# Kernel optimization log

Measured on AMD Instinct MI355X. Metric: run time of the kernel, lower is better.

The kernel has to match this reference:

```python
import jax, jax.numpy as jnp
import numpy as np

MARGIN = 1.0


def _rand_offdiag(key, n):
    # uniform random index j != k for each row k (replaces Python random.choice)
    j = jax.random.randint(key, (n,), 0, n - 1)
    return j + (j >= jnp.arange(n)).astype(j.dtype)


def _semi_hard_margin_loss(logits, j_rand, j_fallback, margin):
    # logits: [N, N]; anchor for row k is logits[k, k]
    n = logits.shape[0]
    rows = jnp.arange(n)
    anchor = jnp.diagonal(logits)                      # [N]
    # term 1: random imposter, hinge at 0 (loss added only when diff > 0)
    imp1 = logits[rows, j_rand]
    d1 = jnp.maximum(imp1 - anchor + margin, 0.0)
    # term 2: semi-hard imposter = max over entries strictly below the anchor
    neg_inf = jnp.finfo(logits.dtype).min
    mask = logits < anchor[:, None]                    # diagonal never True
    cand_max = jnp.max(jnp.where(mask, logits, neg_inf), axis=1)
    has_cand = jnp.any(mask, axis=1)
    imp2 = jnp.where(has_cand, cand_max, logits[rows, j_fallback])
    d2 = jnp.maximum(imp2 - anchor + margin, 0.0)
    return jnp.mean(d1 + d2)


def setup_inputs() -> dict:
    key = jax.random.key(0)
    kx, ky = jax.random.split(key)
    x = jax.random.normal(kx, (4096, 1024), dtype=jnp.float32)
    y = jax.random.normal(ky, (4096, 1024), dtype=jnp.float32)
    return {"x": x, "y": y}


def reference(x, y):
    logits = jnp.matmul(x, y.T)                        # [N, N]
    n = logits.shape[0]
    k1, k2, k3, k4 = jax.random.split(jax.random.key(42), 4)
    loss = (_semi_hard_margin_loss(logits, _rand_offdiag(k1, n), _rand_offdiag(k2, n), MARGIN)
            + _semi_hard_margin_loss(logits.T, _rand_offdiag(k3, n), _rand_offdiag(k4, n), MARGIN))
    return loss
```

## Files before the change

kernel.cpp:

```cpp
#include <hip/hip_runtime.h>
#include <stdint.h>
#include <stddef.h>

#define NN 4096
#define KK 1024
#define SPAN 4095u

typedef unsigned short ushort_t;
typedef __attribute__((ext_vector_type(8))) short short8v;
typedef __attribute__((ext_vector_type(4))) float f32x4;

__host__ __device__ inline void tf2x32(uint32_t k0, uint32_t k1,
                                       uint32_t x0, uint32_t x1,
                                       uint32_t* o0, uint32_t* o1) {
  uint32_t ks2 = k0 ^ k1 ^ 0x1BD11BDAu;
  uint32_t v0 = x0 + k0;
  uint32_t v1 = x1 + k1;
#define TF_ROT(x, r) (((x) << (r)) | ((x) >> (32 - (r))))
#define TF_RND(r) do { v0 += v1; v1 = TF_ROT(v1, r); v1 ^= v0; } while (0)
  TF_RND(13); TF_RND(15); TF_RND(26); TF_RND(6);
  v0 += k1;  v1 += ks2 + 1u;
  TF_RND(17); TF_RND(29); TF_RND(16); TF_RND(24);
  v0 += ks2; v1 += k0 + 2u;
  TF_RND(13); TF_RND(15); TF_RND(26); TF_RND(6);
  v0 += k0;  v1 += k1 + 3u;
  TF_RND(17); TF_RND(29); TF_RND(16); TF_RND(24);
  v0 += k1;  v1 += ks2 + 4u;
  TF_RND(13); TF_RND(15); TF_RND(26); TF_RND(6);
  v0 += ks2; v1 += k0 + 5u;
#undef TF_RND
#undef TF_ROT
  *o0 = v0; *o1 = v1;
}

__device__ inline uint32_t rb32(uint32_t ka, uint32_t kb, uint32_t i) {
  uint32_t a, b;
  tf2x32(ka, kb, 0u, i, &a, &b);
  return a ^ b;
}

__device__ inline uint32_t fenc(float f) {
  uint32_t b = __float_as_uint(f);
  return (b & 0x80000000u) ? ~b : (b | 0x80000000u);
}
__device__ inline float fdec(uint32_t e) {
  uint32_t b = (e & 0x80000000u) ? (e & 0x7FFFFFFFu) : ~e;
  return __uint_as_float(b);
}

__device__ inline ushort_t bf16rne(float f) {
  uint32_t u = __float_as_uint(f);
  return (ushort_t)((u + 0x7FFFu + ((u >> 16) & 1u)) >> 16);
}

__device__ inline void glds16(const void* g, void* l) {
  __builtin_amdgcn_global_load_lds((const __attribute__((address_space(1))) void*)g,
                                   (__attribute__((address_space(3))) void*)l, 16, 0, 0);
}

__global__ __launch_bounds__(256) void k_front(
    const float* __restrict__ X, const float* __restrict__ Y,
    ushort_t* __restrict__ Xb, ushort_t* __restrict__ Yb,
    uint32_t s0a, uint32_t s0b, uint32_t s1a, uint32_t s1b,
    uint32_t s2a, uint32_t s2b, uint32_t s3a, uint32_t s3b,
    uint32_t* __restrict__ rowmax, uint32_t* __restrict__ colmax,
    float* __restrict__ anchor, float* __restrict__ irr, float* __restrict__ irf,
    float* __restrict__ icr, float* __restrict__ icf) {
  const int b = blockIdx.x, tid = threadIdx.x;

  if (b < 4096) {
    if (b < 16) rowmax[b * 256 + tid] = 0u;
    else if (b < 32) colmax[(b - 16) * 256 + tid] = 0u;
    const float4* src = (const float4*)((b < 2048) ? X : Y);
    ushort4* dst = (ushort4*)((b < 2048) ? Xb : Yb);
    const int n4 = NN * KK / 4;
    for (int i = (b & 2047) * 256 + tid; i < n4; i += 2048 * 256) {
      float4 v = src[i];
      ushort4 o;
      o.x = bf16rne(v.x); o.y = bf16rne(v.y); o.z = bf16rne(v.z); o.w = bf16rne(v.w);
      dst[i] = o;
    }
    return;
  }

  const int wid = tid >> 6;
  const int lane = tid & 63;
  const int row = (b - 4096) * 4 + wid;

  int jl = 0;
  if (lane < 4) {
    uint32_t ka = (lane == 0) ? s0a : (lane == 1) ? s1a : (lane == 2) ? s2a : s3a;
    uint32_t kb = (lane == 0) ? s0b : (lane == 1) ? s1b : (lane == 2) ? s2b : s3b;
    uint32_t k1a, k1b, k2a, k2b;
    tf2x32(ka, kb, 0u, 0u, &k1a, &k1b);
    tf2x32(ka, kb, 0u, 1u, &k2a, &k2b);
    uint32_t hi = rb32(k1a, k1b, (uint32_t)row);
    uint32_t lo = rb32(k2a, k2b, (uint32_t)row);
    uint32_t off = ((hi % SPAN) * 256u + (lo % SPAN)) % SPAN;
    int j = (int)off;
    jl = j + ((j >= row) ? 1 : 0);
  }
  const int j1r = __shfl(jl, 0), j1f = __shfl(jl, 1);
  const int j2r = __shfl(jl, 2), j2f = __shfl(jl, 3);

  const float4* xk = (const float4*)(X + (size_t)row * KK);
  const float4* yk = (const float4*)(Y + (size_t)row * KK);
  const float4* y1 = (const float4*)(Y + (size_t)j1r * KK);
  const float4* y2 = (const float4*)(Y + (size_t)j1f * KK);
  const float4* x1 = (const float4*)(X + (size_t)j2r * KK);
  const float4* x2 = (const float4*)(X + (size_t)j2f * KK);
  float sa = 0.f, s1 = 0.f, s2 = 0.f, s3 = 0.f, s4 = 0.f;
  for (int t = lane; t < KK / 4; t += 64) {
    float4 xv = xk[t], yv = yk[t], a1 = y1[t], a2 = y2[t], b1 = x1[t], b2 = x2[t];
    sa = fmaf(xv.x, yv.x, fmaf(xv.y, yv.y, fmaf(xv.z, yv.z, fmaf(xv.w, yv.w, sa))));
    s1 = fmaf(xv.x, a1.x, fmaf(xv.y, a1.y, fmaf(xv.z, a1.z, fmaf(xv.w, a1.w, s1))));
    s2 = fmaf(xv.x, a2.x, fmaf(xv.y, a2.y, fmaf(xv.z, a2.z, fmaf(xv.w, a2.w, s2))));
    s3 = fmaf(b1.x, yv.x, fmaf(b1.y, yv.y, fmaf(b1.z, yv.z, fmaf(b1.w, yv.w, s3))));
    s4 = fmaf(b2.x, yv.x, fmaf(b2.y, yv.y, fmaf(b2.z, yv.z, fmaf(b2.w, yv.w, s4))));
  }
  for (int m = 32; m >= 1; m >>= 1) {
    sa += __shfl_xor(sa, m);
    s1 += __shfl_xor(s1, m);
    s2 += __shfl_xor(s2, m);
    s3 += __shfl_xor(s3, m);
    s4 += __shfl_xor(s4, m);
  }
  if (lane == 0) {
    anchor[row] = sa; irr[row] = s1; irf[row] = s2; icr[row] = s3; icf[row] = s4;
  }
}

__global__ __launch_bounds__(512, 2) void k_gemm8p(
    const ushort_t* __restrict__ A, const ushort_t* __restrict__ B,
    const float* __restrict__ anchor,
    uint32_t* __restrict__ rowmax, uint32_t* __restrict__ colmax) {
  __shared__ ushort_t AL[2][2][8192];
  __shared__ ushort_t BL[2][2][8192];

  const int tid = threadIdx.x;
  const int lane = tid & 63;
  const int w = tid >> 6, wr = w >> 2, wc = w & 3;
  const int l15 = lane & 15, l4 = lane >> 4;

  const int swz = (blockIdx.x & 7) * 32 + (blockIdx.x >> 3);
  const int bi = swz >> 4, bj = swz & 15;

  const int strow = tid >> 3;
  const int scol = ((tid & 7) ^ (strow & 7)) * 8;
  const ushort_t* Abase = A + (size_t)(bi * 256 + strow) * KK + scol;
  const ushort_t* Bbase = B + (size_t)(bj * 256 + strow) * KK + scol;

  const int ss0 = ((0 * 4 + l4) ^ (l15 & 7)) * 8;
  const int ss1 = ((1 * 4 + l4) ^ (l15 & 7)) * 8;
  const int bhalf = wc >> 1, brow0 = (wc & 1) * 64 + l15;

  f32x4 acc[8][4] = {};
  short8v Areg[4][2], B0r[2][2], B1r[2][2];

#define STAGE_A(DD, KT)                                                        \
  do {                                                                         \
    glds16(Abase + (size_t)0 * KK + (KT) * 64,   &AL[DD][0][tid * 8]);         \
    glds16(Abase + (size_t)64 * KK + (KT) * 64,  &AL[DD][0][4096 + tid * 8]);  \
    glds16(Abase + (size_t)128 * KK + (KT) * 64, &AL[DD][1][tid * 8]);         \
    glds16(Abase + (size_t)192 * KK + (KT) * 64, &AL[DD][1][4096 + tid * 8]);  \
  } while (0)
#define STAGE_B(DD, KT)                                                        \
  do {                                                                         \
    glds16(Bbase + (size_t)0 * KK + (KT) * 64,   &BL[DD][0][tid * 8]);         \
    glds16(Bbase + (size_t)64 * KK + (KT) * 64,  &BL[DD][0][4096 + tid * 8]);  \
    glds16(Bbase + (size_t)128 * KK + (KT) * 64, &BL[DD][1][tid * 8]);         \
    glds16(Bbase + (size_t)192 * KK + (KT) * 64, &BL[DD][1][4096 + tid * 8]);  \
  } while (0)

#define BAR() do { __builtin_amdgcn_s_barrier(); \
                   __builtin_amdgcn_sched_barrier(0); } while (0)
#define LGKM0() do { asm volatile("s_waitcnt lgkmcnt(0)" ::: "memory"); \
                     __builtin_amdgcn_sched_barrier(0); } while (0)
#define VM8BAR() do { asm volatile("s_waitcnt vmcnt(8)" ::: "memory"); \
                      __builtin_amdgcn_s_barrier(); \
                      __builtin_amdgcn_sched_barrier(0); } while (0)

#define MFMA1(a, b, c) c = __builtin_amdgcn_mfma_f32_16x16x32_bf16(a, b, c, 0, 0, 0)
#define CL16(MS, NS, BR)                                                       \
  do {                                                                         \
    __builtin_amdgcn_s_setprio(1);                                             \
    _Pragma("unroll")                                                          \
    for (int q = 0; q < 4; ++q) {                                              \
      MFMA1(Areg[q][0], BR[0][0], acc[(MS) * 4 + q][(NS) * 2]);                \
      MFMA1(Areg[q][0], BR[1][0], acc[(MS) * 4 + q][(NS) * 2 + 1]);            \
      MFMA1(Areg[q][1], BR[0][1], acc[(MS) * 4 + q][(NS) * 2]);                \
      MFMA1(Areg[q][1], BR[1][1], acc[(MS) * 4 + q][(NS) * 2 + 1]);            \
    }                                                                          \
    __builtin_amdgcn_s_setprio(0);                                             \
  } while (0)

#define LDA(D, M, KH) (*(const short8v*)&AL[D][wr][((M) * 16 + l15) * 64 + ((KH) ? ss1 : ss0)])
#define LDB(D, N, KH) (*(const short8v*)&BL[D][bhalf][(brow0 + (N) * 16) * 64 + ((KH) ? ss1 : ss0)])

  STAGE_B(0, 0); STAGE_A(0, 0);
  STAGE_B(1, 1); STAGE_A(1, 1);
  asm volatile("s_waitcnt vmcnt(8)" ::: "memory");
  __builtin_amdgcn_s_barrier();
  __builtin_amdgcn_sched_barrier(0);

  for (int i = 0; i < 8; ++i) {
    const int kt2 = (2 * i + 2) & 15, kt3 = (2 * i + 3) & 15;

#pragma unroll
    for (int q = 0; q < 4; ++q) { Areg[q][0] = LDA(0, q, 0); Areg[q][1] = LDA(0, q, 1); }
#pragma unroll
    for (int n = 0; n < 2; ++n) { B0r[n][0] = LDB(0, n, 0); B0r[n][1] = LDB(0, n, 1); }
    BAR(); LGKM0();
    CL16(0, 0, B0r);
    BAR();

#pragma unroll
    for (int n = 0; n < 2; ++n) { B1r[n][0] = LDB(0, n + 2, 0); B1r[n][1] = LDB(0, n + 2, 1); }
    BAR(); LGKM0();
    CL16(0, 1, B1r);
    BAR();

#pragma unroll
    for (int q = 0; q < 4; ++q) { Areg[q][0] = LDA(0, q + 4, 0); Areg[q][1] = LDA(0, q + 4, 1); }
    STAGE_B(0, kt2);
    BAR(); LGKM0();
    CL16(1, 1, B1r);
    BAR();

    STAGE_A(0, kt2);
    BAR(); LGKM0();
    CL16(1, 0, B0r);
    VM8BAR();

#pragma unroll
    for (int q = 0; q < 4; ++q) { Areg[q][0] = LDA(1, q, 0); Areg[q][1] = LDA(1, q, 1); }
#pragma unroll
    for (int n = 0; n < 2; ++n) { B0r[n][0] = LDB(1, n, 0); B0r[n][1] = LDB(1, n, 1); }
    BAR(); LGKM0();
    CL16(0, 0, B0r);
    BAR();

#pragma unroll
    for (int n = 0; n < 2; ++n) { B1r[n][0] = LDB(1, n + 2, 0); B1r[n][1] = LDB(1, n + 2, 1); }
    BAR(); LGKM0();
    CL16(0, 1, B1r);
    BAR();

#pragma unroll
    for (int q = 0; q < 4; ++q) { Areg[q][0] = LDA(1, q + 4, 0); Areg[q][1] = LDA(1, q + 4, 1); }
    STAGE_B(1, kt3);
    BAR(); LGKM0();
    CL16(1, 1, B1r);
    BAR();

    STAGE_A(1, kt3);
    BAR(); LGKM0();
    CL16(1, 0, B0r);
    VM8BAR();
  }

#undef LDA
#undef LDB
#undef CL16
#undef MFMA1
#undef VM8BAR
#undef LGKM0
#undef BAR
#undef STAGE_A
#undef STAGE_B

  const int rbase = bi * 256 + wr * 128;
  const int cbase = bj * 256 + wc * 64;

  float ar[32], ac[4];
#pragma unroll
  for (int m = 0; m < 8; ++m)
#pragma unroll
    for (int r = 0; r < 4; ++r)
      ar[m * 4 + r] = anchor[rbase + m * 16 + l4 * 4 + r];
#pragma unroll
  for (int n = 0; n < 4; ++n)
    ac[n] = anchor[cbase + n * 16 + l15];

#pragma unroll
  for (int m = 0; m < 8; ++m) {
#pragma unroll
    for (int r = 0; r < 4; ++r) {
      const int rg = rbase + m * 16 + l4 * 4 + r;
      const float a = ar[m * 4 + r];
      uint32_t e = 0;
#pragma unroll
      for (int n = 0; n < 4; ++n) {
        const int cg = cbase + n * 16 + l15;
        float v = acc[m][n][r];
        if (v < a && rg != cg) { uint32_t fe = fenc(v); e = (fe > e) ? fe : e; }
      }
#pragma unroll
      for (int sh = 1; sh < 16; sh <<= 1) {
        uint32_t o = (uint32_t)__shfl_xor((int)e, sh, 64);
        e = (o > e) ? o : e;
      }
      if (l15 == 0 && e) atomicMax(&rowmax[rg], e);
    }
  }
#pragma unroll
  for (int n = 0; n < 4; ++n) {
    const int cg = cbase + n * 16 + l15;
    const float a = ac[n];
    uint32_t e = 0;
#pragma unroll
    for (int m = 0; m < 8; ++m) {
#pragma unroll
      for (int r = 0; r < 4; ++r) {
        const int rg = rbase + m * 16 + l4 * 4 + r;
        float v = acc[m][n][r];
        if (v < a && rg != cg) { uint32_t fe = fenc(v); e = (fe > e) ? fe : e; }
      }
    }
    {
      uint32_t o = (uint32_t)__shfl_xor((int)e, 16, 64); e = (o > e) ? o : e;
      o = (uint32_t)__shfl_xor((int)e, 32, 64);          e = (o > e) ? o : e;
    }
    if (l4 == 0 && e) atomicMax(&colmax[cg], e);
  }
}

__global__ __launch_bounds__(256) void k_final(
    const float* __restrict__ anchor,
    const float* __restrict__ irr, const float* __restrict__ irf,
    const float* __restrict__ icr, const float* __restrict__ icf,
    const uint32_t* __restrict__ rowmax, const uint32_t* __restrict__ colmax,
    float* __restrict__ out) {
  float s = 0.f;
  for (int k = (int)threadIdx.x; k < NN; k += 256) {
    float a = anchor[k];
    float d1 = fmaxf(irr[k] - a + 1.0f, 0.f);
    uint32_t rm = rowmax[k];
    float imp2r = rm ? fdec(rm) : irf[k];
    float d2 = fmaxf(imp2r - a + 1.0f, 0.f);
    float e1 = fmaxf(icr[k] - a + 1.0f, 0.f);
    uint32_t cm = colmax[k];
    float imp2c = cm ? fdec(cm) : icf[k];
    float e2 = fmaxf(imp2c - a + 1.0f, 0.f);
    s += d1 + d2 + e1 + e2;
  }
  __shared__ float red[4];
  for (int m = 32; m >= 1; m >>= 1) s += __shfl_xor(s, m);
  if ((threadIdx.x & 63) == 0) red[threadIdx.x >> 6] = s;
  __syncthreads();
  if (threadIdx.x == 0) out[0] = (red[0] + red[1] + red[2] + red[3]) * (1.0f / NN);
}

extern "C" void kernel_launch(void* const* d_in, const int* in_sizes, int n_in,
                              void* d_out, int out_size, void* d_ws, size_t ws_size,
                              hipStream_t stream) {
  const float* X = (const float*)d_in[0];
  const float* Y = (const float*)d_in[1];
  float* out = (float*)d_out;

  char* ws = (char*)d_ws;
  float* anchor    = (float*)(ws + 0 * 16384);
  float* irr       = (float*)(ws + 1 * 16384);
  float* irf       = (float*)(ws + 2 * 16384);
  float* icr       = (float*)(ws + 3 * 16384);
  float* icf       = (float*)(ws + 4 * 16384);
  uint32_t* rowmax = (uint32_t*)(ws + 5 * 16384);
  uint32_t* colmax = (uint32_t*)(ws + 6 * 16384);
  ushort_t* Xb     = (ushort_t*)(ws + 256 * 1024);
  ushort_t* Yb     = Xb + (size_t)NN * KK;

  uint32_t sk[4][2];
  for (int i = 0; i < 4; ++i) tf2x32(0u, 42u, 0u, (uint32_t)i, &sk[i][0], &sk[i][1]);

  k_front<<<4096 + NN / 4, 256, 0, stream>>>(
      X, Y, Xb, Yb,
      sk[0][0], sk[0][1], sk[1][0], sk[1][1], sk[2][0], sk[2][1], sk[3][0], sk[3][1],
      rowmax, colmax, anchor, irr, irf, icr, icf);

  k_gemm8p<<<256, 512, 0, stream>>>(Xb, Yb, anchor, rowmax, colmax);

  k_final<<<1, 256, 0, stream>>>(anchor, irr, irf, icr, icf, rowmax, colmax, out);
}
```

Baseline: 94.20 us.

## Use four waves per 256x256 tile with 128x128 per-wave subtiles

The GEMM block drops from 512 threads (8 waves, each computing 128x64) to 256 threads (4 waves, each computing 128x128), with correspondingly more staging loads per thread and a restructured per-k-tile MFMA schedule. Each wave now holds 64 accumulator tiles and reuses each A and B fragment across more MFMAs, which reduces LDS reads per flop. In exchange, register pressure roughly doubles, occupancy drops to one block with four waves per CU, and there are fewer waves available to hide latency.

Result: slower. 141.5 us (+50.2%).

```diff
diff --git a/kernel.cpp b/kernel.cpp
--- a/kernel.cpp
+++ b/kernel.cpp
@@ -130,7 +130,7 @@
   }
 }
 
-__global__ __launch_bounds__(512, 2) void k_gemm8p(
+__global__ __launch_bounds__(256, 1) void k_gemm4w(
     const ushort_t* __restrict__ A, const ushort_t* __restrict__ B,
     const float* __restrict__ anchor,
     uint32_t* __restrict__ rowmax, uint32_t* __restrict__ colmax) {
@@ -139,7 +139,7 @@
 
   const int tid = threadIdx.x;
   const int lane = tid & 63;
-  const int w = tid >> 6, wr = w >> 2, wc = w & 3;
+  const int w = tid >> 6, wr = w >> 1, wc = w & 1;
   const int l15 = lane & 15, l4 = lane >> 4;
 
   const int swz = (blockIdx.x & 7) * 32 + (blockIdx.x >> 3);
@@ -147,139 +147,131 @@
 
   const int strow = tid >> 3;
   const int scol = ((tid & 7) ^ (strow & 7)) * 8;
-  const ushort_t* Abase = A + (size_t)(bi * 256 + strow) * KK + scol;
-  const ushort_t* Bbase = B + (size_t)(bj * 256 + strow) * KK + scol;
+  const ushort_t* Ab0 = A + (size_t)(bi * 256 + strow) * KK + scol;
+  const ushort_t* Ab1 = A + (size_t)(bi * 256 + 128 + strow) * KK + scol;
+  const ushort_t* Bb0 = B + (size_t)(bj * 256 + strow) * KK + scol;
+  const ushort_t* Bb1 = B + (size_t)(bj * 256 + 128 + strow) * KK + scol;
 
   const int ss0 = ((0 * 4 + l4) ^ (l15 & 7)) * 8;
   const int ss1 = ((1 * 4 + l4) ^ (l15 & 7)) * 8;
-  const int bhalf = wc >> 1, brow0 = (wc & 1) * 64 + l15;
-
-  f32x4 acc[8][4] = {};
-  short8v Areg[4][2], B0r[2][2], B1r[2][2];
+
+  f32x4 acc[8][8] = {};
+  short8v Areg[8], B0r[4], B1r[4];
 
 #define STAGE_A(DD, KT)                                                        \
   do {                                                                         \
-    glds16(Abase + (size_t)0 * KK + (KT) * 64,   &AL[DD][0][tid * 8]);         \
-    glds16(Abase + (size_t)64 * KK + (KT) * 64,  &AL[DD][0][4096 + tid * 8]);  \
-    glds16(Abase + (size_t)128 * KK + (KT) * 64, &AL[DD][1][tid * 8]);         \
-    glds16(Abase + (size_t)192 * KK + (KT) * 64, &AL[DD][1][4096 + tid * 8]);  \
+    glds16(Ab0 + (size_t)0 * KK + (KT) * 64,   &AL[DD][0][0 * 2048 + tid * 8]);\
+    glds16(Ab0 + (size_t)32 * KK + (KT) * 64,  &AL[DD][0][1 * 2048 + tid * 8]);\
+    glds16(Ab0 + (size_t)64 * KK + (KT) * 64,  &AL[DD][0][2 * 2048 + tid * 8]);\
+    glds16(Ab0 + (size_t)96 * KK + (KT) * 64,  &AL[DD][0][3 * 2048 + tid * 8]);\
+    glds16(Ab1 + (size_t)0 * KK + (KT) * 64,   &AL[DD][1][0 * 2048 + tid * 8]);\
+    glds16(Ab1 + (size_t)32 * KK + (KT) * 64,  &AL[DD][1][1 * 2048 + tid * 8]);\
+    glds16(Ab1 + (size_t)64 * KK + (KT) * 64,  &AL[DD][1][2 * 2048 + tid * 8]);\
+    glds16(Ab1 + (size_t)96 * KK + (KT) * 64,  &AL[DD][1][3 * 2048 + tid * 8]);\
   } while (0)
 #define STAGE_B(DD, KT)                                                        \
   do {                                                                         \
-    glds16(Bbase + (size_t)0 * KK + (KT) * 64,   &BL[DD][0][tid * 8]);         \
-    glds16(Bbase + (size_t)64 * KK + (KT) * 64,  &BL[DD][0][4096 + tid * 8]);  \
-    glds16(Bbase + (size_t)128 * KK + (KT) * 64, &BL[DD][1][tid * 8]);         \
-    glds16(Bbase + (size_t)192 * KK + (KT) * 64, &BL[DD][1][4096 + tid * 8]);  \
+    glds16(Bb0 + (size_t)0 * KK + (KT) * 64,   &BL[DD][0][0 * 2048 + tid * 8]);\
+    glds16(Bb0 + (size_t)32 * KK + (KT) * 64,  &BL[DD][0][1 * 2048 + tid * 8]);\
+    glds16(Bb0 + (size_t)64 * KK + (KT) * 64,  &BL[DD][0][2 * 2048 + tid * 8]);\
+    glds16(Bb0 + (size_t)96 * KK + (KT) * 64,  &BL[DD][0][3 * 2048 + tid * 8]);\
+    glds16(Bb1 + (size_t)0 * KK + (KT) * 64,   &BL[DD][1][0 * 2048 + tid * 8]);\
+    glds16(Bb1 + (size_t)32 * KK + (KT) * 64,  &BL[DD][1][1 * 2048 + tid * 8]);\
+    glds16(Bb1 + (size_t)64 * KK + (KT) * 64,  &BL[DD][1][2 * 2048 + tid * 8]);\
+    glds16(Bb1 + (size_t)96 * KK + (KT) * 64,  &BL[DD][1][3 * 2048 + tid * 8]);\
   } while (0)
 
 #define BAR() do { __builtin_amdgcn_s_barrier(); \
                    __builtin_amdgcn_sched_barrier(0); } while (0)
 #define LGKM0() do { asm volatile("s_waitcnt lgkmcnt(0)" ::: "memory"); \
                      __builtin_amdgcn_sched_barrier(0); } while (0)
-#define VM8BAR() do { asm volatile("s_waitcnt vmcnt(8)" ::: "memory"); \
-                      __builtin_amdgcn_s_barrier(); \
-                      __builtin_amdgcn_sched_barrier(0); } while (0)
+#define VM16BAR() do { asm volatile("s_waitcnt vmcnt(16)" ::: "memory"); \
+                       __builtin_amdgcn_s_barrier(); \
+                       __builtin_amdgcn_sched_barrier(0); } while (0)
+
+#define RD_A(D, KH)                                                            \
+  do {                                                                         \
+    _Pragma("unroll")                                                          \
+    for (int q = 0; q < 8; ++q)                                                \
+      Areg[q] = *(const short8v*)&AL[D][wr][(q * 16 + l15) * 64                \
+                                            + ((KH) ? ss1 : ss0)];             \
+  } while (0)
+#define RD_B(RR, D, NB, KH)                                                    \
+  do {                                                                         \
+    _Pragma("unroll")                                                          \
+    for (int n = 0; n < 4; ++n)                                                \
+      RR[n] = *(const short8v*)&BL[D][wc][(((NB) * 4 + n) * 16 + l15) * 64     \
+                                          + ((KH) ? ss1 : ss0)];               \
+  } while (0)
 
 #define MFMA1(a, b, c) c = __builtin_amdgcn_mfma_f32_16x16x32_bf16(a, b, c, 0, 0, 0)
-#define CL16(MS, NS, BR)                                                       \
+#define CL32(BR, NB)                                                           \
   do {                                                                         \
     __builtin_amdgcn_s_setprio(1);                                             \
     _Pragma("unroll")                                                          \
-    for (int q = 0; q < 4; ++q) {                                              \
-      MFMA1(Areg[q][0], BR[0][0], acc[(MS) * 4 + q][(NS) * 2]);                \
-      MFMA1(Areg[q][0], BR[1][0], acc[(MS) * 4 + q][(NS) * 2 + 1]);            \
-      MFMA1(Areg[q][1], BR[0][1], acc[(MS) * 4 + q][(NS) * 2]);                \
-      MFMA1(Areg[q][1], BR[1][1], acc[(MS) * 4 + q][(NS) * 2 + 1]);            \
+    for (int q = 0; q < 8; ++q) {                                              \
+      MFMA1(Areg[q], BR[0], acc[q][(NB) * 4 + 0]);                             \
+      MFMA1(Areg[q], BR[1], acc[q][(NB) * 4 + 1]);                             \
+      MFMA1(Areg[q], BR[2], acc[q][(NB) * 4 + 2]);                             \
+      MFMA1(Areg[q], BR[3], acc[q][(NB) * 4 + 3]);                             \
     }                                                                          \
     __builtin_amdgcn_s_setprio(0);                                             \
   } while (0)
 
-#define LDA(D, M, KH) (*(const short8v*)&AL[D][wr][((M) * 16 + l15) * 64 + ((KH) ? ss1 : ss0)])
-#define LDB(D, N, KH) (*(const short8v*)&BL[D][bhalf][(brow0 + (N) * 16) * 64 + ((KH) ? ss1 : ss0)])
+#define KTILE(D, KT)                                                           \
+  do {                                                                         \
+    RD_A(D, 0); RD_B(B0r, D, 0, 0);                                            \
+    BAR(); LGKM0();                                                            \
+    CL32(B0r, 0);                                                              \
+    BAR();                                                                     \
+    RD_B(B1r, D, 1, 0);                                                        \
+    BAR(); LGKM0();                                                            \
+    CL32(B1r, 1);                                                              \
+    BAR();                                                                     \
+    RD_A(D, 1); RD_B(B0r, D, 0, 1); RD_B(B1r, D, 1, 1);                        \
+    BAR(); LGKM0();                                                            \
+    CL32(B0r, 0);                                                              \
+    BAR();                                                                     \
+    STAGE_B(D, KT); STAGE_A(D, KT);                                            \
+    BAR();                                                                     \
+    CL32(B1r, 1);                                                              \
+    VM16BAR();                                                                 \
+  } while (0)
 
   STAGE_B(0, 0); STAGE_A(0, 0);
   STAGE_B(1, 1); STAGE_A(1, 1);
-  asm volatile("s_waitcnt vmcnt(8)" ::: "memory");
+  asm volatile("s_waitcnt vmcnt(16)" ::: "memory");
   __builtin_amdgcn_s_barrier();
   __builtin_amdgcn_sched_barrier(0);
 
   for (int i = 0; i < 8; ++i) {
     const int kt2 = (2 * i + 2) & 15, kt3 = (2 * i + 3) & 15;
-
-#pragma unroll
-    for (int q = 0; q < 4; ++q) { Areg[q][0] = LDA(0, q, 0); Areg[q][1] = LDA(0, q, 1); }
-#pragma unroll
-    for (int n = 0; n < 2; ++n) { B0r[n][0] = LDB(0, n, 0); B0r[n][1] = LDB(0, n, 1); }
-    BAR(); LGKM0();
-    CL16(0, 0, B0r);
-    BAR();
-
-#pragma unroll
-    for (int n = 0; n < 2; ++n) { B1r[n][0] = LDB(0, n + 2, 0); B1r[n][1] = LDB(0, n + 2, 1); }
-    BAR(); LGKM0();
-    CL16(0, 1, B1r);
-    BAR();
-
-#pragma unroll
-    for (int q = 0; q < 4; ++q) { Areg[q][0] = LDA(0, q + 4, 0); Areg[q][1] = LDA(0, q + 4, 1); }
-    STAGE_B(0, kt2);
-    BAR(); LGKM0();
-    CL16(1, 1, B1r);
-    BAR();
-
-    STAGE_A(0, kt2);
-    BAR(); LGKM0();
-    CL16(1, 0, B0r);
-    VM8BAR();
-
-#pragma unroll
-    for (int q = 0; q < 4; ++q) { Areg[q][0] = LDA(1, q, 0); Areg[q][1] = LDA(1, q, 1); }
-#pragma unroll
-    for (int n = 0; n < 2; ++n) { B0r[n][0] = LDB(1, n, 0); B0r[n][1] = LDB(1, n, 1); }
-    BAR(); LGKM0();
-    CL16(0, 0, B0r);
-    BAR();
-
-#pragma unroll
-    for (int n = 0; n < 2; ++n) { B1r[n][0] = LDB(1, n + 2, 0); B1r[n][1] = LDB(1, n + 2, 1); }
-    BAR(); LGKM0();
-    CL16(0, 1, B1r);
-    BAR();
-
-#pragma unroll
-    for (int q = 0; q < 4; ++q) { Areg[q][0] = LDA(1, q + 4, 0); Areg[q][1] = LDA(1, q + 4, 1); }
-    STAGE_B(1, kt3);
-    BAR(); LGKM0();
-    CL16(1, 1, B1r);
-    BAR();
-
-    STAGE_A(1, kt3);
-    BAR(); LGKM0();
-    CL16(1, 0, B0r);
-    VM8BAR();
-  }
-
-#undef LDA
-#undef LDB
-#undef CL16
+    KTILE(0, kt2);
+    KTILE(1, kt3);
+  }
+
+#undef KTILE
+#undef CL32
 #undef MFMA1
-#undef VM8BAR
+#undef RD_B
+#undef RD_A
+#undef VM16BAR
 #undef LGKM0
 #undef BAR
+#undef STAGE_B
 #undef STAGE_A
-#undef STAGE_B
 
   const int rbase = bi * 256 + wr * 128;
-  const int cbase = bj * 256 + wc * 64;
-
-  float ar[32], ac[4];
+  const int cbase = bj * 256 + wc * 128;
+
+  float ar[32], ac[8];
 #pragma unroll
   for (int m = 0; m < 8; ++m)
 #pragma unroll
     for (int r = 0; r < 4; ++r)
       ar[m * 4 + r] = anchor[rbase + m * 16 + l4 * 4 + r];
 #pragma unroll
-  for (int n = 0; n < 4; ++n)
+  for (int n = 0; n < 8; ++n)
     ac[n] = anchor[cbase + n * 16 + l15];
 
 #pragma unroll
@@ -290,7 +282,7 @@
       const float a = ar[m * 4 + r];
       uint32_t e = 0;
 #pragma unroll
-      for (int n = 0; n < 4; ++n) {
+      for (int n = 0; n < 8; ++n) {
         const int cg = cbase + n * 16 + l15;
         float v = acc[m][n][r];
         if (v < a && rg != cg) { uint32_t fe = fenc(v); e = (fe > e) ? fe : e; }
@@ -304,7 +296,7 @@
     }
   }
 #pragma unroll
-  for (int n = 0; n < 4; ++n) {
+  for (int n = 0; n < 8; ++n) {
     const int cg = cbase + n * 16 + l15;
     const float a = ac[n];
     uint32_t e = 0;
@@ -377,7 +369,7 @@
       sk[0][0], sk[0][1], sk[1][0], sk[1][1], sk[2][0], sk[2][1], sk[3][0], sk[3][1],
       rowmax, colmax, anchor, irr, irf, icr, icf);
 
-  k_gemm8p<<<256, 512, 0, stream>>>(Xb, Yb, anchor, rowmax, colmax);
+  k_gemm4w<<<256, 256, 0, stream>>>(Xb, Yb, anchor, rowmax, colmax);
 
   k_final<<<1, 256, 0, stream>>>(anchor, irr, irf, icr, icf, rowmax, colmax, out);
 }
```
